# Kernel optimization log

Hardware: AMD Instinct MI355X
Metric: run time of the kernel (lower is better)

Reference implementation:

```python
import jax, jax.numpy as jnp
import numpy as np
import math

B, S, D, H = 8, 1024, 512, 8
AD = D // H  # attn_dim = 64


def setup_inputs() -> dict:
    key = jax.random.key(0)
    ks = jax.random.split(key, 16)
    def lin(i):
        w = jax.random.normal(ks[i], (D, D), jnp.float32) * (1.0 / math.sqrt(D))
        b = jnp.zeros((D,), jnp.float32)
        return w, b
    Wq, bq = lin(0); Wk, bk = lin(1); Wv, bv = lin(2); Wr, br = lin(3); Wo, bo = lin(4)
    return {
        "query": jax.random.normal(ks[5], (B, S, D), jnp.float32),
        "key": jax.random.normal(ks[6], (B, S, D), jnp.float32),
        "value": jax.random.normal(ks[7], (B, S, D), jnp.float32),
        "relpos": jax.random.normal(ks[8], (B, S, D), jnp.float32),
        "key_padding_mask": jnp.zeros((B, S), dtype=bool),
        "Wq": Wq, "bq": bq, "Wk": Wk, "bk": bk, "Wv": Wv, "bv": bv,
        "Wr": Wr, "br": br, "Wo": Wo, "bo": bo,
        "U_bias": jax.random.normal(ks[9], (H, AD), jnp.float32) * 0.05,
        "V_bias": jax.random.normal(ks[10], (H, AD), jnp.float32) * 0.05,
    }


def _rel_shift(x):
    # x: (b, h, q, k). Transformer-XL shift trick.
    b, h, q, k = x.shape
    xp = jnp.pad(x, ((0, 0), (0, 0), (0, 0), (1, 0)))  # (b,h,q,k+1)
    xp = xp.reshape(b, h, k + 1, q)
    return xp[:, :, 1:].reshape(b, h, q, k)


def reference(query, key, value, relpos, key_padding_mask,
              Wq, bq, Wk, bk, Wv, bv, Wr, br, Wo, bo, U_bias, V_bias):
    b = query.shape[0]
    Q = (query @ Wq.T + bq).reshape(b, -1, H, AD)    # (b,q,h,d)
    K = (key @ Wk.T + bk).reshape(b, -1, H, AD)      # (b,k,h,d)
    V = (value @ Wv.T + bv).reshape(b, -1, H, AD)    # (b,k,h,d)
    R = (relpos @ Wr.T + br).reshape(b, -1, H, AD)   # (b,k,h,d)

    AC = jnp.einsum('bqhd,bkhd->bhqk', Q + U_bias, K)
    BD = _rel_shift(jnp.einsum('bqhd,bkhd->bhqk', Q + V_bias, R))
    scores = (AC + BD) / math.sqrt(AD)               # (b,h,q,k)

    bias = jnp.where(key_padding_mask, jnp.float32(-1e9), jnp.float32(0.0))
    scores = scores + bias[:, None, None, :]
    attn = jax.nn.softmax(scores, axis=-1)           # (b,h,q,k)

    Hc = jnp.einsum('bhqk,bkhd->bqhd', attn, V).reshape(b, -1, D)
    out = Hc @ Wo.T + bo
    attn_weights = attn.reshape(b * H, attn.shape[2], attn.shape[3])
    return out, attn_weights
```

## Files before the change

kernel.cpp:

```cpp
#include <hip/hip_runtime.h>


typedef __attribute__((ext_vector_type(8))) short bf16x8;
typedef __attribute__((ext_vector_type(8))) float f32x8;
typedef __attribute__((ext_vector_type(4))) float f32x4;

#define MFMA16(a, b, c) __builtin_amdgcn_mfma_f32_16x16x32_bf16((a), (b), (c), 0, 0, 0)

__device__ __forceinline__ float b2f(short s) {
    union { unsigned u; float f; } v;
    v.u = ((unsigned)(unsigned short)s) << 16;
    return v.f;
}
__device__ __forceinline__ short f2b(float f) {
    union { float f; unsigned u; } v;
    v.f = f;
    unsigned r = v.u + 0x7fffu + ((v.u >> 16) & 1u);
    return (short)(r >> 16);
}
__device__ __forceinline__ bf16x8 ld8(const void* p, long idx, int isbf) {
    if (isbf) return *(const bf16x8*)((const short*)p + idx);
    f32x8 f = *(const f32x8*)((const float*)p + idx);
    bf16x8 r;
#pragma unroll
    for (int j = 0; j < 8; j++) r[j] = f2b(f[j]);
    return r;
}
__device__ __forceinline__ float ld1(const void* p, long idx, int isbf) {
    return isbf ? b2f(((const short*)p)[idx]) : ((const float*)p)[idx];
}

__global__ void sniff_dtype(const unsigned* __restrict__ q, int* __restrict__ flag) {
    if (threadIdx.x == 0 && blockIdx.x == 0) {
        int hits = 0;
        for (int i = 0; i < 64; i++) {
            unsigned e = (q[i] >> 7) & 0xFFu;
            hits += (e >= 100u && e <= 140u) ? 1 : 0;
        }
        *flag = (hits > 40) ? 1 : 0;
    }
}

struct CvtArgs { const void* src[8]; };
__global__ __launch_bounds__(256) void convert_all(
        CvtArgs a, short* __restrict__ dst, const int* __restrict__ flag) {
    const int isbf = *flag;
    const long NP = 4194304, WN = 262144;
    const int bid = blockIdx.x;
    int seg;
    long dstoff, eoff;
    if (bid < 8192) {
        seg = bid >> 11;
        dstoff = (long)seg * NP;
        eoff = (long)(bid & 2047) * 2048 + threadIdx.x * 8;
    } else {
        seg = 4 + ((bid - 8192) >> 7);
        dstoff = 4 * NP + (long)(seg - 4) * WN;
        eoff = (long)((bid - 8192) & 127) * 2048 + threadIdx.x * 8;
    }
    const void* s = a.src[seg];
    if (isbf) {
        *(bf16x8*)(dst + dstoff + eoff) = *(const bf16x8*)((const short*)s + eoff);
    } else {
        f32x8 f = *(const f32x8*)((const float*)s + eoff);
        bf16x8 r;
#pragma unroll
        for (int j = 0; j < 8; j++) r[j] = f2b(f[j]);
        *(bf16x8*)(dst + dstoff + eoff) = r;
    }
}

__device__ __forceinline__ void gemm_body(
        const short* __restrict__ A, const void* __restrict__ W,
        const void* __restrict__ bias, void* __restrict__ C,
        int bm, int bn, int isbf, int w_isbf, int c_f32) {
    const int w = threadIdx.x >> 6, lane = threadIdx.x & 63;
    const int m0 = bm * 128 + (w >> 1) * 64;
    const int n0 = bn * 128 + (w & 1) * 64;
    const int lr = lane & 15, lk8 = (lane >> 4) * 8;

    f32x4 acc[4][4] = {};
    for (int kk = 0; kk < 512; kk += 32) {
        bf16x8 a[4], bfr[4];
#pragma unroll
        for (int r = 0; r < 4; r++)
            a[r] = *(const bf16x8*)(A + (long)(m0 + r * 16 + lr) * 512 + kk + lk8);
#pragma unroll
        for (int c = 0; c < 4; c++)
            bfr[c] = ld8(W, (long)(n0 + c * 16 + lr) * 512 + kk + lk8, w_isbf);
#pragma unroll
        for (int r = 0; r < 4; r++)
#pragma unroll
            for (int c = 0; c < 4; c++)
                acc[r][c] = MFMA16(a[r], bfr[c], acc[r][c]);
    }
    const int orow = (lane >> 4) * 4;
#pragma unroll
    for (int c = 0; c < 4; c++) {
        const int col = n0 + c * 16 + lr;
        const float bv = ld1(bias, col, isbf);
#pragma unroll
        for (int r = 0; r < 4; r++)
#pragma unroll
            for (int j = 0; j < 4; j++) {
                const long off = (long)(m0 + r * 16 + orow + j) * 512 + col;
                const float v = acc[r][c][j] + bv;
                if (c_f32) ((float*)C)[off] = v;
                else       ((short*)C)[off] = f2b(v);
            }
    }
}

__global__ __launch_bounds__(256) void gemm_xwT(
        const short* __restrict__ A, const void* __restrict__ W,
        const void* __restrict__ bias, void* __restrict__ C,
        const int* __restrict__ flag, int w_dyn, int c_f32) {
    const int isbf = *flag;
    gemm_body(A, W, bias, C, blockIdx.x & 63, blockIdx.x >> 6,
              isbf, w_dyn ? isbf : 1, c_f32);
}

struct P4 { const void* bias[4]; short* C[4]; };
__global__ __launch_bounds__(256) void proj4(
        const short* __restrict__ Sc, P4 p4, const int* __restrict__ flag) {
    const int isbf = *flag;
    const long NP = 4194304, WN = 262144;
    const int p = blockIdx.x;
    const int xcd = p & 7, u = p >> 3;
    const int op = xcd >> 1;
    const int idx = (xcd & 1) * 128 + u;
    gemm_body(Sc + (long)op * NP, Sc + 4 * NP + (long)op * WN,
              p4.bias[op], p4.C[op], idx & 63, idx >> 6, isbf, 1, 0);
}

__global__ __launch_bounds__(256) void transpose_v(
        const short* __restrict__ Vp, short* __restrict__ Vt) {
    __shared__ short T[64][72];
    const int bh = blockIdx.x >> 2;
    const int kq = blockIdx.x & 3;
    const int b = bh >> 3, h = bh & 7;
    const int t = threadIdx.x;
    const short* src = Vp + (long)b * 1024 * 512 + h * 64;
    short* dst = Vt + (long)bh * 65536;
    for (int kb = kq * 4; kb < kq * 4 + 4; kb++) {
        __syncthreads();
#pragma unroll
        for (int it = 0; it < 2; it++) {
            const int row = it * 32 + (t >> 3);
            const int col = (t & 7) * 8;
            *(bf16x8*)&T[row][col] =
                *(const bf16x8*)(src + (long)(kb * 64 + row) * 512 + col);
        }
        __syncthreads();
#pragma unroll
        for (int it = 0; it < 2; it++) {
            const int d = it * 32 + (t >> 3);
            const int kk = (t & 7) * 8;
            bf16x8 v;
#pragma unroll
            for (int e = 0; e < 8; e++) v[e] = T[kk + e][d];
            *(bf16x8*)(dst + (long)d * 1024 + kb * 64 + kk) = v;
        }
    }
}

__global__ __launch_bounds__(256, 4) void attn_fused(
        const short* __restrict__ Q, const short* __restrict__ K,
        const short* __restrict__ R, const short* __restrict__ Vt,
        const void* __restrict__ Ub, const void* __restrict__ Vb,
        const unsigned char* __restrict__ mask,
        float* __restrict__ attn_out, short* __restrict__ Hc,
        const int* __restrict__ flag) {
    __shared__ __align__(16) short Esh[17 * 1032];
    __shared__ float redmx[4][16];
    __shared__ float redsm[4][16];
    const int isbf = *flag;

    const int p = blockIdx.x;
    const int xcd = p & 7, u = p >> 3;
    const int bh = (u >> 6) * 8 + xcd;
    const int qt = u & 63;
    const int b = bh >> 3, h = bh & 7;
    const int q0 = qt * 16;
    const int w = threadIdx.x >> 6, lane = threadIdx.x & 63;
    const int lr = lane & 15, lg = lane >> 4, lk8 = lg * 8;

    const long kvbase = (long)(b * 1024) * 512 + h * 64;

    {
        bf16x8 aV0[2], aV1[2];
#pragma unroll
        for (int ks = 0; ks < 2; ks++) {
            const int dof = ks * 32 + lk8;
            bf16x8 qv = *(const bf16x8*)(Q + (long)(b * 1024 + q0 + lr) * 512 + h * 64 + dof);
            int qr = q0 + 16 + lr;
            if (qr > 1023) qr = 1023;
            bf16x8 qv1 = *(const bf16x8*)(Q + (long)(b * 1024 + qr) * 512 + h * 64 + dof);
#pragma unroll
            for (int j = 0; j < 8; j++) {
                const float vbj = ld1(Vb, h * 64 + dof + j, isbf);
                aV0[ks][j] = f2b(b2f(qv[j]) + vbj);
                aV1[ks][j] = f2b(b2f(qv1[j]) + vbj);
            }
        }
#pragma unroll 4
        for (int tt = 0; tt < 16; tt++) {
            const int k0 = (w * 16 + tt) * 16;
            f32x4 e0 = {}, e1 = {};
#pragma unroll
            for (int ks = 0; ks < 2; ks++) {
                bf16x8 rf = *(const bf16x8*)(R + kvbase + (long)(k0 + lr) * 512 + ks * 32 + lk8);
                e0 = MFMA16(aV0[ks], rf, e0);
                e1 = MFMA16(aV1[ks], rf, e1);
            }
            const int jcol = k0 + lr;
#pragma unroll
            for (int j = 0; j < 4; j++)
                Esh[(lg * 4 + j) * 1032 + jcol] = f2b(e0[j]);
            if (lg == 0) Esh[16 * 1032 + jcol] = f2b(e1[0]);
        }
    }
    __syncthreads();

    f32x4 acc[16];
    {
        bf16x8 aU[2];
#pragma unroll
        for (int ks = 0; ks < 2; ks++) {
            const int dof = ks * 32 + lk8;
            bf16x8 qv = *(const bf16x8*)(Q + (long)(b * 1024 + q0 + lr) * 512 + h * 64 + dof);
#pragma unroll
            for (int j = 0; j < 8; j++)
                aU[ks][j] = f2b(b2f(qv[j]) + ld1(Ub, h * 64 + dof + j, isbf));
        }
        const unsigned char* mrow = mask + b * 1024;
#pragma unroll
        for (int tt = 0; tt < 16; tt++) {
            const int k0 = (w * 16 + tt) * 16;
            f32x4 a = {};
#pragma unroll
            for (int ks = 0; ks < 2; ks++) {
                bf16x8 kf = *(const bf16x8*)(K + kvbase + (long)(k0 + lr) * 512 + ks * 32 + lk8);
                a = MFMA16(aU[ks], kf, a);
            }
            const int c = k0 + lr;
            const float mbias = mrow[c] ? -1e9f : 0.0f;
#pragma unroll
            for (int j = 0; j < 4; j++) {
                const int r = lg * 4 + j;
                const int dq = c - q0 - r;
                const int idx = r * 1032 + dq + ((dq <= 0) ? 1023 : 1030);
                float bd = b2f(Esh[idx]);
                if (dq == 1) bd = 0.0f;
                a[j] = (a[j] + bd) * 0.125f + mbias;
            }
            acc[tt] = a;
        }
    }

    float mx[4], sm[4];
#pragma unroll
    for (int j = 0; j < 4; j++) {
        float m = -1e30f;
#pragma unroll
        for (int tt = 0; tt < 16; tt++) m = fmaxf(m, acc[tt][j]);
#pragma unroll
        for (int off = 1; off <= 8; off <<= 1) m = fmaxf(m, __shfl_xor(m, off));
        mx[j] = m;
    }
    if (lr == 0) {
#pragma unroll
        for (int j = 0; j < 4; j++) redmx[w][lg * 4 + j] = mx[j];
    }
    __syncthreads();
#pragma unroll
    for (int j = 0; j < 4; j++) {
        float m = redmx[0][lg * 4 + j];
#pragma unroll
        for (int ww = 1; ww < 4; ww++) m = fmaxf(m, redmx[ww][lg * 4 + j]);
        mx[j] = m;
        sm[j] = 0.0f;
    }
#pragma unroll
    for (int tt = 0; tt < 16; tt++)
#pragma unroll
        for (int j = 0; j < 4; j++) {
            const float e = __expf(acc[tt][j] - mx[j]);
            acc[tt][j] = e;
            sm[j] += e;
        }
#pragma unroll
    for (int j = 0; j < 4; j++) {
#pragma unroll
        for (int off = 1; off <= 8; off <<= 1) sm[j] += __shfl_xor(sm[j], off);
    }
    if (lr == 0) {
#pragma unroll
        for (int j = 0; j < 4; j++) redsm[w][lg * 4 + j] = sm[j];
    }
    __syncthreads();
    float inv[4];
#pragma unroll
    for (int j = 0; j < 4; j++) {
        float s = redsm[0][lg * 4 + j];
#pragma unroll
        for (int ww = 1; ww < 4; ww++) s += redsm[ww][lg * 4 + j];
        inv[j] = 1.0f / s;
    }

    short* P = Esh;
#pragma unroll
    for (int tt = 0; tt < 16; tt++) {
        const int c = (w * 16 + tt) * 16 + lr;
#pragma unroll
        for (int j = 0; j < 4; j++)
            P[(lg * 4 + j) * 1048 + c] = f2b(acc[tt][j] * inv[j]);
    }
    __syncthreads();

    float* abase = attn_out + ((long)bh * 1024 + q0) * 1024;
#pragma unroll
    for (int rr = 0; rr < 4; rr++) {
        const int r = w * 4 + rr;
#pragma unroll
        for (int half = 0; half < 2; half++) {
            const bf16x8 pv8 = *(const bf16x8*)&P[r * 1048 + half * 512 + lane * 8];
            f32x4 lo, hi;
#pragma unroll
            for (int e = 0; e < 4; e++) { lo[e] = b2f(pv8[e]); hi[e] = b2f(pv8[4 + e]); }
            float* dst = abase + (long)r * 1024 + half * 512 + lane * 8;
            *(f32x4*)dst = lo;
            *(f32x4*)(dst + 4) = hi;
        }
    }

    f32x4 oacc = {};
    const short* vtb = Vt + (long)bh * 65536 + (long)(w * 16 + lr) * 1024;
    for (int ks = 0; ks < 32; ks++) {
        const bf16x8 aa = *(const bf16x8*)&P[lr * 1048 + ks * 32 + lk8];
        const bf16x8 bb = *(const bf16x8*)(vtb + ks * 32 + lk8);
        oacc = MFMA16(aa, bb, oacc);
    }
#pragma unroll
    for (int j = 0; j < 4; j++)
        Hc[(long)(b * 1024 + q0 + lg * 4 + j) * 512 + h * 64 + w * 16 + lr] = f2b(oacc[j]);
}

extern "C" void kernel_launch(void* const* d_in, const int* in_sizes, int n_in,
                              void* d_out, int out_size, void* d_ws, size_t ws_size,
                              hipStream_t stream) {
    const void* query  = d_in[0];
    const void* key    = d_in[1];
    const void* value  = d_in[2];
    const void* relpos = d_in[3];
    const unsigned char* mask = (const unsigned char*)d_in[4];
    const void* Wq = d_in[5];  const void* bq = d_in[6];
    const void* Wk = d_in[7];  const void* bk = d_in[8];
    const void* Wv = d_in[9];  const void* bv = d_in[10];
    const void* Wr = d_in[11]; const void* br = d_in[12];
    const void* Wo = d_in[13]; const void* bo = d_in[14];
    const void* Ub = d_in[15]; const void* Vb = d_in[16];

    float* out  = (float*)d_out;
    float* attn = out + (long)4194304;

    const long NP = 4194304;
    short* ws = (short*)d_ws;
    short* Kp = ws;
    short* Vp = ws + NP;
    short* Rp = ws + 2 * NP;
    int* flag = (int*)(ws + 3 * NP);
    short* Qp = (short*)out;
    short* Vt = (short*)out + NP;
    short* Hc = Vp;
    short* Sc = (short*)attn;

    sniff_dtype<<<1, 64, 0, stream>>>((const unsigned*)query, flag);

    CvtArgs ca;
    ca.src[0] = query; ca.src[1] = key; ca.src[2] = value; ca.src[3] = relpos;
    ca.src[4] = Wq; ca.src[5] = Wk; ca.src[6] = Wv; ca.src[7] = Wr;
    convert_all<<<8704, 256, 0, stream>>>(ca, Sc, flag);

    P4 p4;
    p4.bias[0] = bq; p4.C[0] = Qp;
    p4.bias[1] = bk; p4.C[1] = Kp;
    p4.bias[2] = bv; p4.C[2] = Vp;
    p4.bias[3] = br; p4.C[3] = Rp;
    proj4<<<1024, 256, 0, stream>>>(Sc, p4, flag);

    transpose_v<<<256, 256, 0, stream>>>(Vp, Vt);

    attn_fused<<<4096, 256, 0, stream>>>(Qp, Kp, Rp, Vt, Ub, Vb, mask,
                                         attn, Hc, flag);

    gemm_xwT<<<256, 256, 0, stream>>>(Hc, Wo, bo, out, flag, 1, 1);
}
```

Measured before the change: 365.4 us.

## Pack two query tiles per attention block and use smaller output GEMM tiles

The attention kernel now runs 512 threads per block, with two independent 4-wave groups each handling a 16-row query tile, which halves the grid. Shared memory doubles to hold one score buffer per group. The final output projection moves to a new kernel with 64x64 tiles and 1024 blocks, replacing 256 blocks of 128x128, to fill more compute units. gemm_body gains an A-dtype parameter that is not used for new behaviour. The cost is more LDS per block, which may reduce occupancy, and block-wide syncs that now span both groups.

```diff
diff --git a/kernel.cpp b/kernel.cpp
--- a/kernel.cpp
+++ b/kernel.cpp
@@ -71,9 +71,9 @@
 }
 
 __device__ __forceinline__ void gemm_body(
-        const short* __restrict__ A, const void* __restrict__ W,
+        const void* __restrict__ A, const void* __restrict__ W,
         const void* __restrict__ bias, void* __restrict__ C,
-        int bm, int bn, int isbf, int w_isbf, int c_f32) {
+        int bm, int bn, int isbf, int a_isbf, int w_isbf, int c_f32) {
     const int w = threadIdx.x >> 6, lane = threadIdx.x & 63;
     const int m0 = bm * 128 + (w >> 1) * 64;
     const int n0 = bn * 128 + (w & 1) * 64;
@@ -84,7 +84,7 @@
         bf16x8 a[4], bfr[4];
 #pragma unroll
         for (int r = 0; r < 4; r++)
-            a[r] = *(const bf16x8*)(A + (long)(m0 + r * 16 + lr) * 512 + kk + lk8);
+            a[r] = ld8(A, (long)(m0 + r * 16 + lr) * 512 + kk + lk8, a_isbf);
 #pragma unroll
         for (int c = 0; c < 4; c++)
             bfr[c] = ld8(W, (long)(n0 + c * 16 + lr) * 512 + kk + lk8, w_isbf);
@@ -109,15 +109,6 @@
                 else       ((short*)C)[off] = f2b(v);
             }
     }
-}
-
-__global__ __launch_bounds__(256) void gemm_xwT(
-        const short* __restrict__ A, const void* __restrict__ W,
-        const void* __restrict__ bias, void* __restrict__ C,
-        const int* __restrict__ flag, int w_dyn, int c_f32) {
-    const int isbf = *flag;
-    gemm_body(A, W, bias, C, blockIdx.x & 63, blockIdx.x >> 6,
-              isbf, w_dyn ? isbf : 1, c_f32);
 }
 
 struct P4 { const void* bias[4]; short* C[4]; };
@@ -130,7 +121,42 @@
     const int op = xcd >> 1;
     const int idx = (xcd & 1) * 128 + u;
     gemm_body(Sc + (long)op * NP, Sc + 4 * NP + (long)op * WN,
-              p4.bias[op], p4.C[op], idx & 63, idx >> 6, isbf, 1, 0);
+              p4.bias[op], p4.C[op], idx & 63, idx >> 6, isbf, 1, 1, 0);
+}
+
+__global__ __launch_bounds__(256) void gemm_xwT64(
+        const short* __restrict__ A, const void* __restrict__ W,
+        const void* __restrict__ bias, float* __restrict__ C,
+        const int* __restrict__ flag, int w_dyn) {
+    const int isbf = *flag;
+    const int w_isbf = w_dyn ? isbf : 1;
+    const int bm = blockIdx.x & 127;
+    const int bn = blockIdx.x >> 7;
+    const int w = threadIdx.x >> 6, lane = threadIdx.x & 63;
+    const int m0 = bm * 64 + w * 16;
+    const int n0 = bn * 64;
+    const int lr = lane & 15, lk8 = (lane >> 4) * 8;
+
+    f32x4 acc[4] = {};
+    for (int kk = 0; kk < 512; kk += 32) {
+        bf16x8 a = *(const bf16x8*)(A + (long)(m0 + lr) * 512 + kk + lk8);
+        bf16x8 bfr[4];
+#pragma unroll
+        for (int c = 0; c < 4; c++)
+            bfr[c] = ld8(W, (long)(n0 + c * 16 + lr) * 512 + kk + lk8, w_isbf);
+#pragma unroll
+        for (int c = 0; c < 4; c++)
+            acc[c] = MFMA16(a, bfr[c], acc[c]);
+    }
+    const int orow = (lane >> 4) * 4;
+#pragma unroll
+    for (int c = 0; c < 4; c++) {
+        const int col = n0 + c * 16 + lr;
+        const float bv = ld1(bias, col, isbf);
+#pragma unroll
+        for (int j = 0; j < 4; j++)
+            C[(long)(m0 + orow + j) * 512 + col] = acc[c][j] + bv;
+    }
 }
 
 __global__ __launch_bounds__(256) void transpose_v(
@@ -164,36 +190,39 @@
     }
 }
 
-__global__ __launch_bounds__(256, 4) void attn_fused(
+__global__ __launch_bounds__(512, 4) void attn_fused(
         const short* __restrict__ Q, const short* __restrict__ K,
         const short* __restrict__ R, const short* __restrict__ Vt,
         const void* __restrict__ Ub, const void* __restrict__ Vb,
         const unsigned char* __restrict__ mask,
         float* __restrict__ attn_out, short* __restrict__ Hc,
         const int* __restrict__ flag) {
-    __shared__ __align__(16) short Esh[17 * 1032];
-    __shared__ float redmx[4][16];
-    __shared__ float redsm[4][16];
+    __shared__ __align__(16) short Esh[2][17 * 1032];
+    __shared__ float redmx[2][4][16];
+    __shared__ float redsm[2][4][16];
     const int isbf = *flag;
 
     const int p = blockIdx.x;
     const int xcd = p & 7, u = p >> 3;
-    const int bh = (u >> 6) * 8 + xcd;
-    const int qt = u & 63;
+    const int bh = (u >> 5) * 8 + xcd;
+    const int qt = u & 31;
     const int b = bh >> 3, h = bh & 7;
-    const int q0 = qt * 16;
+    const int q0 = qt * 32;
     const int w = threadIdx.x >> 6, lane = threadIdx.x & 63;
+    const int g = w >> 2, wq = w & 3;
+    const int qg0 = q0 + g * 16;
     const int lr = lane & 15, lg = lane >> 4, lk8 = lg * 8;
 
     const long kvbase = (long)(b * 1024) * 512 + h * 64;
+    short* E = &Esh[g][0];
 
     {
         bf16x8 aV0[2], aV1[2];
 #pragma unroll
         for (int ks = 0; ks < 2; ks++) {
             const int dof = ks * 32 + lk8;
-            bf16x8 qv = *(const bf16x8*)(Q + (long)(b * 1024 + q0 + lr) * 512 + h * 64 + dof);
-            int qr = q0 + 16 + lr;
+            bf16x8 qv = *(const bf16x8*)(Q + (long)(b * 1024 + qg0 + lr) * 512 + h * 64 + dof);
+            int qr = qg0 + 16 + lr;
             if (qr > 1023) qr = 1023;
             bf16x8 qv1 = *(const bf16x8*)(Q + (long)(b * 1024 + qr) * 512 + h * 64 + dof);
 #pragma unroll
@@ -205,7 +234,7 @@
         }
 #pragma unroll 4
         for (int tt = 0; tt < 16; tt++) {
-            const int k0 = (w * 16 + tt) * 16;
+            const int k0 = (wq * 16 + tt) * 16;
             f32x4 e0 = {}, e1 = {};
 #pragma unroll
             for (int ks = 0; ks < 2; ks++) {
@@ -216,8 +245,8 @@
             const int jcol = k0 + lr;
 #pragma unroll
             for (int j = 0; j < 4; j++)
-                Esh[(lg * 4 + j) * 1032 + jcol] = f2b(e0[j]);
-            if (lg == 0) Esh[16 * 1032 + jcol] = f2b(e1[0]);
+                E[(lg * 4 + j) * 1032 + jcol] = f2b(e0[j]);
+            if (lg == 0) E[16 * 1032 + jcol] = f2b(e1[0]);
         }
     }
     __syncthreads();
@@ -228,7 +257,7 @@
 #pragma unroll
         for (int ks = 0; ks < 2; ks++) {
             const int dof = ks * 32 + lk8;
-            bf16x8 qv = *(const bf16x8*)(Q + (long)(b * 1024 + q0 + lr) * 512 + h * 64 + dof);
+            bf16x8 qv = *(const bf16x8*)(Q + (long)(b * 1024 + qg0 + lr) * 512 + h * 64 + dof);
 #pragma unroll
             for (int j = 0; j < 8; j++)
                 aU[ks][j] = f2b(b2f(qv[j]) + ld1(Ub, h * 64 + dof + j, isbf));
@@ -236,7 +265,7 @@
         const unsigned char* mrow = mask + b * 1024;
 #pragma unroll
         for (int tt = 0; tt < 16; tt++) {
-            const int k0 = (w * 16 + tt) * 16;
+            const int k0 = (wq * 16 + tt) * 16;
             f32x4 a = {};
 #pragma unroll
             for (int ks = 0; ks < 2; ks++) {
@@ -248,9 +277,9 @@
 #pragma unroll
             for (int j = 0; j < 4; j++) {
                 const int r = lg * 4 + j;
-                const int dq = c - q0 - r;
+                const int dq = c - qg0 - r;
                 const int idx = r * 1032 + dq + ((dq <= 0) ? 1023 : 1030);
-                float bd = b2f(Esh[idx]);
+                float bd = b2f(E[idx]);
                 if (dq == 1) bd = 0.0f;
                 a[j] = (a[j] + bd) * 0.125f + mbias;
             }
@@ -270,14 +299,14 @@
     }
     if (lr == 0) {
 #pragma unroll
-        for (int j = 0; j < 4; j++) redmx[w][lg * 4 + j] = mx[j];
+        for (int j = 0; j < 4; j++) redmx[g][wq][lg * 4 + j] = mx[j];
     }
     __syncthreads();
 #pragma unroll
     for (int j = 0; j < 4; j++) {
-        float m = redmx[0][lg * 4 + j];
-#pragma unroll
-        for (int ww = 1; ww < 4; ww++) m = fmaxf(m, redmx[ww][lg * 4 + j]);
+        float m = redmx[g][0][lg * 4 + j];
+#pragma unroll
+        for (int ww = 1; ww < 4; ww++) m = fmaxf(m, redmx[g][ww][lg * 4 + j]);
         mx[j] = m;
         sm[j] = 0.0f;
     }
@@ -296,32 +325,32 @@
     }
     if (lr == 0) {
 #pragma unroll
-        for (int j = 0; j < 4; j++) redsm[w][lg * 4 + j] = sm[j];
+        for (int j = 0; j < 4; j++) redsm[g][wq][lg * 4 + j] = sm[j];
     }
     __syncthreads();
     float inv[4];
 #pragma unroll
     for (int j = 0; j < 4; j++) {
-        float s = redsm[0][lg * 4 + j];
-#pragma unroll
-        for (int ww = 1; ww < 4; ww++) s += redsm[ww][lg * 4 + j];
+        float s = redsm[g][0][lg * 4 + j];
+#pragma unroll
+        for (int ww = 1; ww < 4; ww++) s += redsm[g][ww][lg * 4 + j];
         inv[j] = 1.0f / s;
     }
 
-    short* P = Esh;
+    short* P = E;
 #pragma unroll
     for (int tt = 0; tt < 16; tt++) {
-        const int c = (w * 16 + tt) * 16 + lr;
+        const int c = (wq * 16 + tt) * 16 + lr;
 #pragma unroll
         for (int j = 0; j < 4; j++)
             P[(lg * 4 + j) * 1048 + c] = f2b(acc[tt][j] * inv[j]);
     }
     __syncthreads();
 
-    float* abase = attn_out + ((long)bh * 1024 + q0) * 1024;
+    float* abase = attn_out + ((long)bh * 1024 + qg0) * 1024;
 #pragma unroll
     for (int rr = 0; rr < 4; rr++) {
-        const int r = w * 4 + rr;
+        const int r = wq * 4 + rr;
 #pragma unroll
         for (int half = 0; half < 2; half++) {
             const bf16x8 pv8 = *(const bf16x8*)&P[r * 1048 + half * 512 + lane * 8];
@@ -335,7 +364,7 @@
     }
 
     f32x4 oacc = {};
-    const short* vtb = Vt + (long)bh * 65536 + (long)(w * 16 + lr) * 1024;
+    const short* vtb = Vt + (long)bh * 65536 + (long)(wq * 16 + lr) * 1024;
     for (int ks = 0; ks < 32; ks++) {
         const bf16x8 aa = *(const bf16x8*)&P[lr * 1048 + ks * 32 + lk8];
         const bf16x8 bb = *(const bf16x8*)(vtb + ks * 32 + lk8);
@@ -343,7 +372,7 @@
     }
 #pragma unroll
     for (int j = 0; j < 4; j++)
-        Hc[(long)(b * 1024 + q0 + lg * 4 + j) * 512 + h * 64 + w * 16 + lr] = f2b(oacc[j]);
+        Hc[(long)(b * 1024 + qg0 + lg * 4 + j) * 512 + h * 64 + wq * 16 + lr] = f2b(oacc[j]);
 }
 
 extern "C" void kernel_launch(void* const* d_in, const int* in_sizes, int n_in,
@@ -391,8 +420,8 @@
 
     transpose_v<<<256, 256, 0, stream>>>(Vp, Vt);
 
-    attn_fused<<<4096, 256, 0, stream>>>(Qp, Kp, Rp, Vt, Ub, Vb, mask,
+    attn_fused<<<2048, 512, 0, stream>>>(Qp, Kp, Rp, Vt, Ub, Vb, mask,
                                          attn, Hc, flag);
 
-    gemm_xwT<<<256, 256, 0, stream>>>(Hc, Wo, bo, out, flag, 1, 1);
-}
+    gemm_xwT64<<<1024, 256, 0, stream>>>(Hc, Wo, bo, out, flag, 1);
+}
```

New measurement: 386.2 us. 5.7% more time.
